# Performance work log

Measured on AMD Instinct MI355X. Metric: run time of the kernel, lower is better.

The kernel has to match this reference:

```python
import jax, jax.numpy as jnp
import numpy as np


def log_g(x):
    # log of the 'continuous' g: g(x) = x + 0.5 for x>=0, sigmoid(x) otherwise
    return jnp.where(x >= 0, jnp.log(jax.nn.relu(x) + 0.5), -jax.nn.softplus(-x))


def setup_inputs() -> dict:
    key = jax.random.key(0)
    ks = jax.random.split(key, 6)
    B, T, D, H = 8, 4096, 1024, 1024
    s = 1.0 / np.sqrt(D)
    return {
        "x": jax.random.normal(ks[0], (B, T, D), dtype=jnp.float32),
        "h_0": jax.random.uniform(ks[1], (B, 1, H), dtype=jnp.float32),
        "Wz": jax.random.normal(ks[2], (D, H), dtype=jnp.float32) * s,
        "bz": jnp.zeros((H,), dtype=jnp.float32),
        "Wh": jax.random.normal(ks[3], (D, H), dtype=jnp.float32) * s,
        "bh": jnp.zeros((H,), dtype=jnp.float32),
    }


def reference(x, h_0, Wz, bz, Wh, bh):
    # x: [B,T,D], h_0: [B,1,H]
    k = jnp.einsum('btd,dh->bth', x, Wz) + bz            # gate pre-activation
    log_z = -jax.nn.softplus(-k)                          # log sigmoid(k)
    log_coeffs = -jax.nn.softplus(k)                      # log (1 - sigmoid(k))
    log_h0 = log_g(h_0)                                   # [B,1,H]
    log_tilde_h = log_g(jnp.einsum('btd,dh->bth', x, Wh) + bh)
    # parallel scan in log space over time axis
    a_star = jnp.pad(jnp.cumsum(log_coeffs, axis=1), ((0, 0), (1, 0), (0, 0)))  # [B,T+1,H]
    log_values = jnp.concatenate([log_h0, log_z + log_tilde_h], axis=1)          # [B,T+1,H]
    log_h = a_star + jax.lax.cumlogsumexp(log_values - a_star, axis=1)
    return jnp.exp(log_h)  # [B,T+1,H]
```

## Files before the change

### kernel.cpp

```cpp
#include <hip/hip_runtime.h>
#include <hip/hip_bf16.h>
#include <cstdint>
#include <cstddef>

#define B_ 8
#define T_ 4096
#define D_ 1024
#define H_ 1024
#define M_ (B_*T_)
#define NCHUNK 64
#define CLEN 64

using bf16x8   = __attribute__((ext_vector_type(8))) __bf16;
using floatx4  = __attribute__((ext_vector_type(4))) float;
using float4v  = __attribute__((ext_vector_type(4))) float;
using float2v  = __attribute__((ext_vector_type(2))) float;
using ushort4v = __attribute__((ext_vector_type(4))) unsigned short;
using aw2_t    = __attribute__((ext_vector_type(2))) _Float16;
using halfx4   = __attribute__((ext_vector_type(4))) _Float16;
using halfx8   = __attribute__((ext_vector_type(8))) _Float16;

__device__ inline unsigned short f2bf(float f) {
  union { float f; unsigned u; } v; v.f = f;
  unsigned u = v.u;
  u += 0x7fffu + ((u >> 16) & 1u);
  return (unsigned short)(u >> 16);
}

__device__ inline void async_load16(const void* g, void* l) {
  __builtin_amdgcn_global_load_lds((const __attribute__((address_space(1))) void*)g,
                                   (__attribute__((address_space(3))) void*)l,
                                   16, 0, 0);
}

__global__ __launch_bounds__(256) void prep_kernel(const float* __restrict__ x,
                                                   unsigned short* __restrict__ xb,
                                                   const float* __restrict__ Wz,
                                                   const float* __restrict__ Wh,
                                                   unsigned short* __restrict__ Wzt,
                                                   unsigned short* __restrict__ Wht) {
  __shared__ float tile[32][33];
  const int bid = blockIdx.x;
  if (bid < 16384) {
    size_t i = ((size_t)bid * 256 + threadIdx.x) * 2;
#pragma unroll
    for (int j = 0; j < 2; ++j) {
      float4v v = ((const float4v*)x)[i + j];
      ushort4v o = { f2bf(v[0]), f2bf(v[1]), f2bf(v[2]), f2bf(v[3]) };
      ((ushort4v*)xb)[i + j] = o;
    }
  } else {
    const int b2 = bid - 16384;
    const int z = b2 >> 10;
    const int rem = b2 & 1023;
    const int bx = rem & 31, by = rem >> 5;
    const int tx = threadIdx.x & 31, ty = threadIdx.x >> 5;
    const float* W = z ? Wh : Wz;
    unsigned short* Wt = z ? Wht : Wzt;
    const int n0 = bx * 32, k0 = by * 32;
#pragma unroll
    for (int j = 0; j < 4; ++j) {
      int kr = ty + j * 8;
      tile[kr][tx] = W[(size_t)(k0 + kr) * H_ + n0 + tx];
    }
    __syncthreads();
#pragma unroll
    for (int j = 0; j < 4; ++j) {
      int nr = ty + j * 8;
      Wt[(size_t)(n0 + nr) * D_ + k0 + tx] = f2bf(tile[tx][nr]);
    }
  }
}

__global__ __launch_bounds__(256, 2) void gemm_kernel(
    const unsigned short* __restrict__ xb,
    const unsigned short* __restrict__ wzt,
    const unsigned short* __restrict__ wht,
    const float* __restrict__ bz, const float* __restrict__ bh,
    aw2_t* __restrict__ aw_out,
    float* __restrict__ P_ws, float* __restrict__ S_ws) {
  __shared__ __align__(16) unsigned short ldsA[128 * 64];
  __shared__ __align__(16) unsigned short ldsBz[128 * 64];
  __shared__ __align__(16) unsigned short ldsBh[128 * 64];

  const int tid = threadIdx.x;
  const int lane = tid & 63, wid = tid >> 6;
  const int wm = wid >> 1, wn = wid & 1;
  const int row16 = lane & 15, quad = lane >> 4;

  int g = blockIdx.x;
  int x = g & 7, j = g >> 3;
  int n_idx = j & 7;
  int m_idx = (x << 5) | (j >> 3);
  const int m0 = m_idx * 128, n0 = n_idx * 128;

  floatx4 accz[4][4], acch[4][4];
#pragma unroll
  for (int mi = 0; mi < 4; ++mi)
#pragma unroll
    for (int ni = 0; ni < 4; ++ni) {
      accz[mi][ni] = (floatx4){0.f, 0.f, 0.f, 0.f};
      acch[mi][ni] = (floatx4){0.f, 0.f, 0.f, 0.f};
    }

  const int srow = tid >> 3;
  const int jblk = ((tid & 7) - srow) & 7;
  const unsigned short* aSrc  = xb  + (size_t)(m0 + srow) * D_ + jblk * 8;
  const unsigned short* zSrc  = wzt + (size_t)(n0 + srow) * D_ + jblk * 8;
  const unsigned short* hSrc  = wht + (size_t)(n0 + srow) * D_ + jblk * 8;

  const int p0 = (quad + row16) & 7;
  const int p1 = p0 ^ 4;

  for (int kk = 0; kk < D_; kk += 64) {
#pragma unroll
    for (int t = 0; t < 4; ++t) {
      size_t roff = (size_t)(32 * t) * D_ + kk;
      int doff = (tid + 256 * t) * 8;
      async_load16(aSrc + roff, &ldsA[doff]);
      async_load16(zSrc + roff, &ldsBz[doff]);
      async_load16(hSrc + roff, &ldsBh[doff]);
    }
    __syncthreads();

#pragma unroll
    for (int kh = 0; kh < 2; ++kh) {
      const int p = kh ? p1 : p0;
      bf16x8 af[4], bzf[4], bhf[4];
#pragma unroll
      for (int mi = 0; mi < 4; ++mi)
        af[mi] = *(const bf16x8*)&ldsA[(wm * 64 + mi * 16 + row16) * 64 + p * 8];
#pragma unroll
      for (int ni = 0; ni < 4; ++ni) {
        bzf[ni] = *(const bf16x8*)&ldsBz[(wn * 64 + ni * 16 + row16) * 64 + p * 8];
        bhf[ni] = *(const bf16x8*)&ldsBh[(wn * 64 + ni * 16 + row16) * 64 + p * 8];
      }
#pragma unroll
      for (int mi = 0; mi < 4; ++mi)
#pragma unroll
        for (int ni = 0; ni < 4; ++ni) {
          accz[mi][ni] = __builtin_amdgcn_mfma_f32_16x16x32_bf16(af[mi], bzf[ni], accz[mi][ni], 0, 0, 0);
          acch[mi][ni] = __builtin_amdgcn_mfma_f32_16x16x32_bf16(af[mi], bhf[ni], acch[mi][ni], 0, 0, 0);
        }
    }
    __syncthreads();
  }

  const int b_of = m0 >> 12;
  const int cidx = ((m0 & (T_ - 1)) >> 6) + wm;
#pragma unroll
  for (int ni = 0; ni < 4; ++ni) {
    const int col = n0 + wn * 64 + ni * 16 + row16;
    const float bzv = bz[col], bhv = bh[col];
    float Pc = 1.f, Sc = 0.f;
#pragma unroll
    for (int mi = 0; mi < 4; ++mi) {
      float pm = 1.f, sm = 0.f;
#pragma unroll
      for (int r = 0; r < 4; ++r) {
        const int row = m0 + wm * 64 + mi * 16 + quad * 4 + r;
        float k   = accz[mi][ni][r] + bzv;
        float pre = acch[mi][ni][r] + bhv;
        float z  = 1.f / (1.f + __expf(-k));
        float av = 1.f / (1.f + __expf(k));
        float gg = (pre >= 0.f) ? (pre + 0.5f) : 1.f / (1.f + __expf(-pre));
        _Float16 ah = (_Float16)av, wh = (_Float16)(z * gg);
        aw2_t o = { ah, wh };
        aw_out[(size_t)row * H_ + col] = o;
        float afv = (float)ah, wfv = (float)wh;
        sm = afv * sm + wfv;
        pm = afv * pm;
      }
      float pp = __shfl_xor(pm, 16), sp = __shfl_xor(sm, 16);
      sm = (quad & 1) ? (pm * sp + sm) : (pp * sm + sp);
      pm = pm * pp;
      pp = __shfl_xor(pm, 32); sp = __shfl_xor(sm, 32);
      sm = (quad & 2) ? (pm * sp + sm) : (pp * sm + sp);
      pm = pm * pp;
      Sc = pm * Sc + sm;
      Pc = pm * Pc;
    }
    if (quad == 0) {
      size_t o = ((size_t)b_of * H_ + col) * NCHUNK + cidx;
      P_ws[o] = Pc; S_ws[o] = Sc;
    }
  }
}

__global__ __launch_bounds__(256) void scan_pass2(const float* __restrict__ h0,
                                                  const float* __restrict__ P,
                                                  const float* __restrict__ S,
                                                  float* __restrict__ carry,
                                                  float* __restrict__ out) {
  int gid = blockIdx.x * 256 + threadIdx.x;
  int b = gid >> 10, h = gid & 1023;
  float v = h0[(size_t)b * H_ + h];
  float cur = (v >= 0.f) ? (v + 0.5f) : 1.f / (1.f + __expf(-v));
  out[((size_t)b * (T_ + 1)) * H_ + h] = cur;
  const float4v* Pv = (const float4v*)&P[((size_t)b * H_ + h) * NCHUNK];
  const float4v* Sv = (const float4v*)&S[((size_t)b * H_ + h) * NCHUNK];
  float4v* Cv = (float4v*)&carry[((size_t)b * H_ + h) * NCHUNK];
#pragma unroll
  for (int j = 0; j < NCHUNK / 4; ++j) {
    float4v p = Pv[j], s = Sv[j], cc;
    cc[0] = cur; cur = p[0] * cur + s[0];
    cc[1] = cur; cur = p[1] * cur + s[1];
    cc[2] = cur; cur = p[2] * cur + s[2];
    cc[3] = cur; cur = p[3] * cur + s[3];
    Cv[j] = cc;
  }
}

__global__ __launch_bounds__(512) void scan_pass3(const halfx4* __restrict__ aw,
                                                  const float* __restrict__ carry,
                                                  float* __restrict__ out) {
  int c = blockIdx.x;
  int b = blockIdx.y;
  int h2 = threadIdx.x;
  size_t base = (size_t)(b * T_ + c * CLEN) * (H_ / 2) + h2;
  size_t cb = ((size_t)b * H_ + h2 * 2) * NCHUNK + c;
  float c0 = carry[cb], c1 = carry[cb + NCHUNK];
  size_t obase = ((size_t)b * (T_ + 1) + c * CLEN + 1) * (H_ / 2) + h2;
  float2v* outv = (float2v*)out;
#pragma unroll 8
  for (int i = 0; i < CLEN; ++i) {
    halfx4 v = aw[base + (size_t)i * (H_ / 2)];
    c0 = (float)v[0] * c0 + (float)v[1];
    c1 = (float)v[2] * c1 + (float)v[3];
    outv[obase + (size_t)i * (H_ / 2)] = (float2v){c0, c1};
  }
}

extern "C" void kernel_launch(void* const* d_in, const int* in_sizes, int n_in,
                              void* d_out, int out_size, void* d_ws, size_t ws_size,
                              hipStream_t stream) {
  const float* x  = (const float*)d_in[0];
  const float* h0 = (const float*)d_in[1];
  const float* Wz = (const float*)d_in[2];
  const float* bz = (const float*)d_in[3];
  const float* Wh = (const float*)d_in[4];
  const float* bh = (const float*)d_in[5];
  float* out = (float*)d_out;

  char* ws = (char*)d_ws;
  unsigned short* xb  = (unsigned short*)(ws);
  unsigned short* wzt = (unsigned short*)(ws + 67108864ULL);
  unsigned short* wht = (unsigned short*)(ws + 69206016ULL);
  aw2_t* aw_ws = (aw2_t*)(ws + 71303168ULL);
  float* P_ws  = (float*)(ws + 71303168ULL + 134217728ULL);
  float* S_ws  = (float*)(ws + 71303168ULL + 134217728ULL + 2097152ULL);
  float* c_ws  = (float*)(ws + 71303168ULL + 134217728ULL + 2ULL * 2097152ULL);

  hipLaunchKernelGGL(prep_kernel, dim3(16384 + 2048), dim3(256), 0, stream,
                     x, xb, Wz, Wh, wzt, wht);
  hipLaunchKernelGGL(gemm_kernel, dim3(2048), dim3(256), 0, stream,
                     xb, wzt, wht, bz, bh, aw_ws, P_ws, S_ws);
  hipLaunchKernelGGL(scan_pass2, dim3(32), dim3(256), 0, stream, h0, P_ws, S_ws, c_ws, out);
  hipLaunchKernelGGL(scan_pass3, dim3(NCHUNK, B_), dim3(512), 0, stream,
                     (const halfx4*)aw_ws, c_ws, out);
}
```

Before: 462.6 us.

## Fuse chunk-carry scan into final scan pass and transpose P/S layout

Drops the separate serial carry kernel, which ran on only 32 blocks, and instead has each block of the final scan pass recompute its own carry by looping over the preceding chunk summaries. The P/S workspace layout moves to chunk-major with H contiguous, so these reads coalesce across threads. This removes one launch and a poorly parallel serial pass, at the cost of redundant work that grows with the chunk index, giving later chunks more latency.

```diff
diff --git a/kernel.cpp b/kernel.cpp
--- a/kernel.cpp
+++ b/kernel.cpp
@@ -18,7 +18,6 @@
 using ushort4v = __attribute__((ext_vector_type(4))) unsigned short;
 using aw2_t    = __attribute__((ext_vector_type(2))) _Float16;
 using halfx4   = __attribute__((ext_vector_type(4))) _Float16;
-using halfx8   = __attribute__((ext_vector_type(8))) _Float16;
 
 __device__ inline unsigned short f2bf(float f) {
   union { float f; unsigned u; } v; v.f = f;
@@ -181,47 +180,40 @@
       Pc = pm * Pc;
     }
     if (quad == 0) {
-      size_t o = ((size_t)b_of * H_ + col) * NCHUNK + cidx;
+      size_t o = ((size_t)(b_of * NCHUNK + cidx)) * H_ + col;
       P_ws[o] = Pc; S_ws[o] = Sc;
     }
   }
 }
 
-__global__ __launch_bounds__(256) void scan_pass2(const float* __restrict__ h0,
-                                                  const float* __restrict__ P,
-                                                  const float* __restrict__ S,
-                                                  float* __restrict__ carry,
-                                                  float* __restrict__ out) {
-  int gid = blockIdx.x * 256 + threadIdx.x;
-  int b = gid >> 10, h = gid & 1023;
-  float v = h0[(size_t)b * H_ + h];
-  float cur = (v >= 0.f) ? (v + 0.5f) : 1.f / (1.f + __expf(-v));
-  out[((size_t)b * (T_ + 1)) * H_ + h] = cur;
-  const float4v* Pv = (const float4v*)&P[((size_t)b * H_ + h) * NCHUNK];
-  const float4v* Sv = (const float4v*)&S[((size_t)b * H_ + h) * NCHUNK];
-  float4v* Cv = (float4v*)&carry[((size_t)b * H_ + h) * NCHUNK];
-#pragma unroll
-  for (int j = 0; j < NCHUNK / 4; ++j) {
-    float4v p = Pv[j], s = Sv[j], cc;
-    cc[0] = cur; cur = p[0] * cur + s[0];
-    cc[1] = cur; cur = p[1] * cur + s[1];
-    cc[2] = cur; cur = p[2] * cur + s[2];
-    cc[3] = cur; cur = p[3] * cur + s[3];
-    Cv[j] = cc;
-  }
-}
-
-__global__ __launch_bounds__(512) void scan_pass3(const halfx4* __restrict__ aw,
-                                                  const float* __restrict__ carry,
-                                                  float* __restrict__ out) {
-  int c = blockIdx.x;
-  int b = blockIdx.y;
-  int h2 = threadIdx.x;
+__global__ __launch_bounds__(512) void scan_kernel(const halfx4* __restrict__ aw,
+                                                   const float* __restrict__ h0,
+                                                   const float* __restrict__ P,
+                                                   const float* __restrict__ S,
+                                                   float* __restrict__ out) {
+  const int c = blockIdx.x;
+  const int b = blockIdx.y;
+  const int h2 = threadIdx.x;
+  float2v* outv = (float2v*)out;
+
+  const float2v hv = *(const float2v*)&h0[(size_t)b * H_ + 2 * h2];
+  float c0 = (hv[0] >= 0.f) ? (hv[0] + 0.5f) : 1.f / (1.f + __expf(-hv[0]));
+  float c1 = (hv[1] >= 0.f) ? (hv[1] + 0.5f) : 1.f / (1.f + __expf(-hv[1]));
+  if (c == 0)
+    outv[(size_t)b * (T_ + 1) * (H_ / 2) + h2] = (float2v){c0, c1};
+
+  const float2v* Pv = (const float2v*)P;
+  const float2v* Sv = (const float2v*)S;
+  size_t pj = (size_t)b * NCHUNK * (H_ / 2) + h2;
+  for (int j = 0; j < c; ++j) {
+    float2v p = Pv[pj], s = Sv[pj];
+    c0 = p[0] * c0 + s[0];
+    c1 = p[1] * c1 + s[1];
+    pj += H_ / 2;
+  }
+
   size_t base = (size_t)(b * T_ + c * CLEN) * (H_ / 2) + h2;
-  size_t cb = ((size_t)b * H_ + h2 * 2) * NCHUNK + c;
-  float c0 = carry[cb], c1 = carry[cb + NCHUNK];
   size_t obase = ((size_t)b * (T_ + 1) + c * CLEN + 1) * (H_ / 2) + h2;
-  float2v* outv = (float2v*)out;
 #pragma unroll 8
   for (int i = 0; i < CLEN; ++i) {
     halfx4 v = aw[base + (size_t)i * (H_ / 2)];
@@ -249,13 +241,11 @@
   aw2_t* aw_ws = (aw2_t*)(ws + 71303168ULL);
   float* P_ws  = (float*)(ws + 71303168ULL + 134217728ULL);
   float* S_ws  = (float*)(ws + 71303168ULL + 134217728ULL + 2097152ULL);
-  float* c_ws  = (float*)(ws + 71303168ULL + 134217728ULL + 2ULL * 2097152ULL);
 
   hipLaunchKernelGGL(prep_kernel, dim3(16384 + 2048), dim3(256), 0, stream,
                      x, xb, Wz, Wh, wzt, wht);
   hipLaunchKernelGGL(gemm_kernel, dim3(2048), dim3(256), 0, stream,
                      xb, wzt, wht, bz, bh, aw_ws, P_ws, S_ws);
-  hipLaunchKernelGGL(scan_pass2, dim3(32), dim3(256), 0, stream, h0, P_ws, S_ws, c_ws, out);
-  hipLaunchKernelGGL(scan_pass3, dim3(NCHUNK, B_), dim3(512), 0, stream,
-                     (const halfx4*)aw_ws, c_ws, out);
-}
+  hipLaunchKernelGGL(scan_kernel, dim3(NCHUNK, B_), dim3(512), 0, stream,
+                     (const halfx4*)aw_ws, h0, P_ws, S_ws, out);
+}
```

After: 468.7 us. About the same (+1.3%).
